# Kernel optimization log

Hardware: AMD Instinct MI355X
Metric: run time of the kernel (lower is better)

The kernel has to match this reference:

```python
import jax, jax.numpy as jnp
import numpy as np

NUM_HEADS = 16  # matches init_kwargs num_heads


def setup_inputs() -> dict:
    key = jax.random.key(0)
    k0, k1, k2, k3, k4 = jax.random.split(key, 5)
    B, p, C = 8, 64, 1024
    N = p * p
    s = 1.0 / np.sqrt(C).astype(np.float32)
    return {
        "x": jax.random.normal(k0, (B, 3, N, C), jnp.float32),
        "wq": jax.random.normal(k1, (C, C), jnp.float32) * s,
        "wk": jax.random.normal(k2, (C, C), jnp.float32) * s,
        "wv": jax.random.normal(k3, (C, C), jnp.float32) * s,
        "w_proj": jax.random.normal(k4, (C, C), jnp.float32) * s,
        "b_proj": jnp.zeros((C,), jnp.float32),
    }


def reference(x, wq, wk, wv, w_proj, b_proj):
    # x: [B, 3, N, C] triplane tokens, N = p*p
    B, G, N, C = x.shape
    p = int(round(N ** 0.5))
    H = NUM_HEADS
    d = C // H
    scale = d ** -0.5

    xg = x.reshape(B, 3, p, p, C)
    # Linear projections are pointwise, so project each plane element once
    # (the torch code redundantly projects gathered copies; math is identical).
    qh = (xg @ wq.T).reshape(B, 3, p, p, H, d)
    kh = (xg @ wk.T).reshape(B, 3, p, p, H, d)
    vh = (xg @ wv.T).reshape(B, 3, p, p, H, d)

    outs = []
    for i in range(3):  # fixed loop over the 3 planes
        q_i = qh[:, i]                       # [B, a, j, H, d] query pixel (a, j)
        k_yz = kh[:, (i + 1) % 3]            # keys: row a of next plane -> [B, a, k, H, d]
        v_yz = vh[:, (i + 1) % 3]
        k_zx = kh[:, (i + 2) % 3]            # keys: column j of other plane -> [B, k, j, H, d]
        v_zx = vh[:, (i + 2) % 3]
        # scores against the p row-keys and p column-keys (2p keys total, 1 query)
        s1 = jnp.einsum('bajhd,bakhd->bajhk', q_i, k_yz) * scale
        s2 = jnp.einsum('bajhd,bkjhd->bajhk', q_i, k_zx) * scale
        attn = jax.nn.softmax(jnp.concatenate([s1, s2], axis=-1), axis=-1)  # [B,a,j,H,2p]
        a1, a2 = attn[..., :p], attn[..., p:]
        o = (jnp.einsum('bajhk,bakhd->bajhd', a1, v_yz)
             + jnp.einsum('bajhk,bkjhd->bajhd', a2, v_zx))  # [B,a,j,H,d]
        outs.append(o.reshape(B, N, C))
    # torch buffer is filled in [plane, B, N] order then reinterpreted as [B,3,N];
    # replicate that reshape quirk faithfully.
    out = jnp.stack(outs, axis=0)            # [3, B, N, C]
    out = out @ w_proj.T + b_proj
    return out.reshape(B, 3, N, C)
```

## Files before the change

kernel.cpp:

```cpp
#include <hip/hip_runtime.h>
#include <hip/hip_bf16.h>
#include <stdint.h>
#include <type_traits>

typedef __hip_bfloat16 hbf16;
typedef short bf16x8 __attribute__((ext_vector_type(8)));
typedef float f32x4 __attribute__((ext_vector_type(4)));
typedef unsigned int u32x4 __attribute__((ext_vector_type(4)));

#define MFMA16(a, b, c) __builtin_amdgcn_mfma_f32_16x16x32_bf16((a), (b), (c), 0, 0, 0)

__device__ __forceinline__ void gload_lds16(const void* g, void* l) {
  __builtin_amdgcn_global_load_lds(
      (const __attribute__((address_space(1))) void*)g,
      (__attribute__((address_space(3))) void*)l, 16, 0, 0);
}

__device__ __forceinline__ float b2f(unsigned short u) {
  union { unsigned int u32; float f; } cv;
  cv.u32 = ((unsigned int)u) << 16;
  return cv.f;
}
__device__ __forceinline__ unsigned short f2b(float f) {
  hbf16 h = __float2bfloat16(f);
  return __builtin_bit_cast(unsigned short, h);
}

__device__ __forceinline__ int swz(int row, int col) {
  return row * 64 + (col ^ ((row & 7) << 3));
}

__global__ __launch_bounds__(256) void cvt_f32_bf16(
    const float* __restrict__ src, unsigned short* __restrict__ dst, long long n)
{
  const long long i0 = ((long long)blockIdx.x * 256 + threadIdx.x) * 8;
  const long long stride = (long long)gridDim.x * 2048;
  for (long long i = i0; i < n; i += stride) {
    const float4 a = *(const float4*)(src + i);
    const float4 b = *(const float4*)(src + i + 4);
    bf16x8 o;
    o[0] = (short)f2b(a.x); o[1] = (short)f2b(a.y);
    o[2] = (short)f2b(a.z); o[3] = (short)f2b(a.w);
    o[4] = (short)f2b(b.x); o[5] = (short)f2b(b.y);
    o[6] = (short)f2b(b.z); o[7] = (short)f2b(b.w);
    *(bf16x8*)(dst + i) = o;
  }
}

__global__ __launch_bounds__(256) void cvt4_w(
    const float* __restrict__ s0, const float* __restrict__ s1,
    const float* __restrict__ s2, const float* __restrict__ s3,
    unsigned short* __restrict__ dst)
{
  const int q = blockIdx.x >> 9;
  const float* src = (q == 0) ? s0 : (q == 1) ? s1 : (q == 2) ? s2 : s3;
  const long long i = ((long long)(blockIdx.x & 511) * 256 + threadIdx.x) * 8;
  const float4 a = *(const float4*)(src + i);
  const float4 b = *(const float4*)(src + i + 4);
  bf16x8 o;
  o[0] = (short)f2b(a.x); o[1] = (short)f2b(a.y);
  o[2] = (short)f2b(a.z); o[3] = (short)f2b(a.w);
  o[4] = (short)f2b(b.x); o[5] = (short)f2b(b.y);
  o[6] = (short)f2b(b.z); o[7] = (short)f2b(b.w);
  *(bf16x8*)(dst + (long long)q * 1048576 + i) = o;
}

__global__ __launch_bounds__(256, 2) void gemm_qkv(
    const unsigned short* __restrict__ A,
    const unsigned short* __restrict__ W,
    unsigned short* __restrict__ Cq,
    unsigned short* __restrict__ Ck,
    unsigned short* __restrict__ Cv,
    int M, int Ntot, int K)
{
  __shared__ __attribute__((aligned(16))) unsigned short Sm[36864];

  const int tid  = threadIdx.x;
  const int lane = tid & 63;
  const int w    = tid >> 6;
  const int wr   = w >> 1;
  const int wc   = w & 1;
  const int lr   = lane & 15;
  const int lg   = lane >> 4;

  const int bx    = blockIdx.x;
  const int xcd   = bx & 7;
  const int idx   = bx >> 3;
  const int tileN = xcd * 3 + idx % 3;
  const int tileM = idx / 3;
  const size_t rowBase = (size_t)tileM * 256;
  const int    colBase = tileN * 128;

  const int sRow   = tid >> 2;
  const int sChunk = (tid & 3) ^ ((tid >> 3) & 3);
  const unsigned short* Ag0 = A + (rowBase +   0 + sRow) * (size_t)K + sChunk * 8;
  const unsigned short* Ag1 = A + (rowBase +  64 + sRow) * (size_t)K + sChunk * 8;
  const unsigned short* Ag2 = A + (rowBase + 128 + sRow) * (size_t)K + sChunk * 8;
  const unsigned short* Ag3 = A + (rowBase + 192 + sRow) * (size_t)K + sChunk * 8;
  const unsigned short* Wg0 = W + ((size_t)colBase +  0 + sRow) * K + sChunk * 8;
  const unsigned short* Wg1 = W + ((size_t)colBase + 64 + sRow) * K + sChunk * 8;

  f32x4 acc[8][4] = {};
  const int nt = K >> 5;

#pragma unroll
  for (int p = 0; p < 2; ++p) {
    const size_t ke = (size_t)p * 32;
    unsigned short* ab = Sm + p * 8192;
    unsigned short* bb = Sm + 24576 + p * 4096;
    gload_lds16(Ag0 + ke, ab +        w * 512);
    gload_lds16(Ag1 + ke, ab + 2048 + w * 512);
    gload_lds16(Ag2 + ke, ab + 4096 + w * 512);
    gload_lds16(Ag3 + ke, ab + 6144 + w * 512);
    gload_lds16(Wg0 + ke, bb +        w * 512);
    gload_lds16(Wg1 + ke, bb + 2048 + w * 512);
  }

#define QITER(T, VM, STG)                                                     \
  do {                                                                        \
    asm volatile("s_waitcnt vmcnt(" VM ")" ::: "memory");                     \
    __builtin_amdgcn_s_barrier();                                             \
    __builtin_amdgcn_sched_barrier(0);                                        \
    if (STG) {                                                                \
      const int nb = ((T) + 2) % 3;                                           \
      const size_t ke = (size_t)((T) + 2) * 32;                               \
      unsigned short* ab = Sm + nb * 8192;                                    \
      unsigned short* bb = Sm + 24576 + nb * 4096;                            \
      gload_lds16(Ag0 + ke, ab +        w * 512);                             \
      gload_lds16(Ag1 + ke, ab + 2048 + w * 512);                             \
      gload_lds16(Ag2 + ke, ab + 4096 + w * 512);                             \
      gload_lds16(Ag3 + ke, ab + 6144 + w * 512);                             \
      gload_lds16(Wg0 + ke, bb +        w * 512);                             \
      gload_lds16(Wg1 + ke, bb + 2048 + w * 512);                             \
    }                                                                         \
    const unsigned short* asb = Sm + ((T) % 3) * 8192;                        \
    const unsigned short* bsb = Sm + 24576 + ((T) % 3) * 4096;                \
    bf16x8 af[8], bfv[4];                                                     \
    _Pragma("unroll")                                                         \
    for (int mi = 0; mi < 8; ++mi) {                                          \
      const int row = wr * 128 + mi * 16 + lr;                                \
      af[mi] = *(const bf16x8*)(asb + row * 32 + (lg ^ ((row >> 1) & 3)) * 8);\
    }                                                                         \
    _Pragma("unroll")                                                         \
    for (int ni = 0; ni < 4; ++ni) {                                          \
      const int row = wc * 64 + ni * 16 + lr;                                 \
      bfv[ni] = *(const bf16x8*)(bsb + row * 32 + (lg ^ ((row >> 1) & 3)) * 8);\
    }                                                                         \
    _Pragma("unroll")                                                         \
    for (int mi = 0; mi < 8; ++mi)                                            \
      _Pragma("unroll")                                                       \
      for (int ni = 0; ni < 4; ++ni)                                          \
        acc[mi][ni] = MFMA16(af[mi], bfv[ni], acc[mi][ni]);                   \
  } while (0)

  for (int t = 0; t < nt - 2; ++t) QITER(t, "6", true);
  QITER(nt - 2, "6", false);
  QITER(nt - 1, "0", false);
#undef QITER

  __syncthreads();
  unsigned short* G = Sm + wr * 16384;
#pragma unroll
  for (int mi = 0; mi < 8; ++mi)
#pragma unroll
    for (int ni = 0; ni < 4; ++ni)
#pragma unroll
      for (int r = 0; r < 4; ++r) {
        const int row = mi * 16 + lg * 4 + r;
        const int c   = wc * 64 + ni * 16 + lr;
        G[row * 128 + (c ^ (((row >> 2) & 3) << 4))] = f2b(acc[mi][ni][r]);
      }
  __syncthreads();

  const int out = colBase >> 10;
  unsigned short* Co = (out == 0) ? Cq : (out == 1) ? Ck : Cv;
  const int colLocal = colBase & 1023;
#pragma unroll
  for (int it = 0; it < 16; ++it) {
    const int ch  = it * 128 + wc * 64 + lane;
    const int row = ch >> 4, cc = ch & 15;
    const u32x4 v = *(const u32x4*)(G + row * 128 + ((cc * 8) ^ (((row >> 2) & 3) << 4)));
    *(u32x4*)(Co + (rowBase + wr * 128 + row) * 1024 + colLocal + cc * 8) = v;
  }
}

template <typename OutT>
__global__ __launch_bounds__(512, 4) void gemm_bt(
    const unsigned short* __restrict__ A,
    const unsigned short* __restrict__ W,
    const float* __restrict__ bias,
    OutT* __restrict__ C,
    int M, int N, int K)
{
  __shared__ __attribute__((aligned(16))) unsigned short Sm[36864];

  const int tid  = threadIdx.x;
  const int lane = tid & 63;
  const int w    = tid >> 6;
  const int wr64 = (w >> 1) * 64;
  const int wc64 = (w & 1) * 64;
  const int lr   = lane & 15;
  const int lg   = lane >> 4;
  const int wofs = w * 512;

  const int nwg     = gridDim.x;
  const int bx      = blockIdx.x;
  const int logical = (bx & 7) * (nwg >> 3) + (bx >> 3);
  const int colsN   = N >> 7;
  const int tileM   = logical / colsN;
  const int tileN   = logical - tileM * colsN;
  const size_t rowBase = (size_t)tileM * 256;
  const int    colBase = tileN * 128;

  const int sRow   = tid >> 2;
  const int sChunk = (tid & 3) ^ ((tid >> 3) & 3);
  const unsigned short* Ag0 = A + (rowBase + sRow) * (size_t)K + sChunk * 8;
  const unsigned short* Ag1 = Ag0 + (size_t)128 * K;
  const unsigned short* Wg0 = W + ((size_t)colBase + sRow) * K + sChunk * 8;

  f32x4 acc[4][4] = {};
  const int nt = K >> 5;

#pragma unroll
  for (int p = 0; p < 2; ++p) {
    const size_t ke = (size_t)p * 32;
    gload_lds16(Ag0 + ke, Sm + p * 8192 + wofs);
    gload_lds16(Ag1 + ke, Sm + p * 8192 + 4096 + wofs);
    gload_lds16(Wg0 + ke, Sm + 24576 + p * 4096 + wofs);
  }

#define GITER(T, VM, STG)                                                     \
  do {                                                                        \
    asm volatile("s_waitcnt vmcnt(" VM ")" ::: "memory");                     \
    __builtin_amdgcn_s_barrier();                                             \
    __builtin_amdgcn_sched_barrier(0);                                        \
    if (STG) {                                                                \
      const int nb = ((T) + 2) % 3;                                           \
      const size_t ke = (size_t)((T) + 2) * 32;                               \
      gload_lds16(Ag0 + ke, Sm + nb * 8192 + wofs);                           \
      gload_lds16(Ag1 + ke, Sm + nb * 8192 + 4096 + wofs);                    \
      gload_lds16(Wg0 + ke, Sm + 24576 + nb * 4096 + wofs);                   \
    }                                                                         \
    const unsigned short* asb = Sm + ((T) % 3) * 8192;                        \
    const unsigned short* bsb = Sm + 24576 + ((T) % 3) * 4096;                \
    bf16x8 af[4], bfv[4];                                                     \
    _Pragma("unroll")                                                         \
    for (int mi = 0; mi < 4; ++mi) {                                          \
      const int row = wr64 + mi * 16 + lr;                                    \
      af[mi] = *(const bf16x8*)(asb + row * 32 + (lg ^ ((row >> 1) & 3)) * 8);\
    }                                                                         \
    _Pragma("unroll")                                                         \
    for (int ni = 0; ni < 4; ++ni) {                                          \
      const int row = wc64 + ni * 16 + lr;                                    \
      bfv[ni] = *(const bf16x8*)(bsb + row * 32 + (lg ^ ((row >> 1) & 3)) * 8);\
    }                                                                         \
    _Pragma("unroll")                                                         \
    for (int mi = 0; mi < 4; ++mi)                                            \
      _Pragma("unroll")                                                       \
      for (int ni = 0; ni < 4; ++ni)                                          \
        acc[mi][ni] = MFMA16(af[mi], bfv[ni], acc[mi][ni]);                   \
  } while (0)

  for (int t = 0; t < nt - 2; ++t) GITER(t, "3", true);
  GITER(nt - 2, "3", false);
  GITER(nt - 1, "0", false);
#undef GITER

  __syncthreads();

  float bv[4];
#pragma unroll
  for (int ni = 0; ni < 4; ++ni)
    bv[ni] = bias ? bias[colBase + wc64 + ni * 16 + lr] : 0.0f;

  const size_t R0 = rowBase + wr64;
  const int    C0 = colBase + wc64;

#pragma unroll
  for (int batch = 0; batch < 2; ++batch) {
    if constexpr (std::is_same_v<OutT, float>) {
      float* reg = (float*)(void*)Sm + w * 2048;
#pragma unroll
      for (int mi2 = 0; mi2 < 2; ++mi2) {
        const int mi = batch * 2 + mi2;
#pragma unroll
        for (int ni = 0; ni < 4; ++ni)
#pragma unroll
          for (int r = 0; r < 4; ++r) {
            const int row = mi2 * 16 + lg * 4 + r;
            reg[row * 64 + ((ni * 16 + lr) ^ (((row >> 2) & 3) << 4))] =
                acc[mi][ni][r] + bv[ni];
          }
      }
      asm volatile("s_waitcnt lgkmcnt(0)" ::: "memory");
      __builtin_amdgcn_sched_barrier(0);
#pragma unroll
      for (int it = 0; it < 8; ++it) {
        const int ch  = it * 64 + lane;
        const int row = ch >> 4, cc = ch & 15;
        const float4 v = *(const float4*)(reg + row * 64 + ((cc * 4) ^ (((row >> 2) & 3) << 4)));
        *(float4*)((float*)C + (R0 + batch * 32 + row) * (size_t)N + C0 + cc * 4) = v;
      }
    } else {
      unsigned short* reg = Sm + w * 2048;
#pragma unroll
      for (int mi2 = 0; mi2 < 2; ++mi2) {
        const int mi = batch * 2 + mi2;
#pragma unroll
        for (int ni = 0; ni < 4; ++ni)
#pragma unroll
          for (int r = 0; r < 4; ++r)
            reg[(mi2 * 16 + lg * 4 + r) * 64 + ni * 16 + lr] =
                f2b(acc[mi][ni][r] + bv[ni]);
      }
      asm volatile("s_waitcnt lgkmcnt(0)" ::: "memory");
      __builtin_amdgcn_sched_barrier(0);
#pragma unroll
      for (int it = 0; it < 4; ++it) {
        const int ch  = it * 64 + lane;
        const int row = ch >> 3, cc = ch & 7;
        const u32x4 v = *(const u32x4*)(reg + row * 64 + cc * 8);
        *(u32x4*)((unsigned short*)C + (R0 + batch * 32 + row) * (size_t)N + C0 + cc * 8) = v;
      }
    }
  }
}

__global__ __launch_bounds__(256) void attn_yz(
    const unsigned short* __restrict__ Q,
    const unsigned short* __restrict__ Kx,
    const unsigned short* __restrict__ Vx,
    unsigned short* __restrict__ O1,
    float* __restrict__ m1s, float* __restrict__ l1s)
{
  __shared__ __attribute__((aligned(16))) unsigned short Qs[4096], Ks[4096], Vs[4096], Ps[4096];

  const int bid = blockIdx.x;
  const int h = bid & 15;
  const int a = (bid >> 4) & 63;
  const int b = (bid >> 10) & 7;
  const int i = bid >> 13;
  const int i1 = (i + 1) % 3;

  const size_t qoff = ((size_t)((b * 3 + i) * 4096 + a * 64)) * 1024 + h * 64;
  const size_t koff = ((size_t)((b * 3 + i1) * 4096 + a * 64)) * 1024 + h * 64;

  const int tid = threadIdx.x;
#pragma unroll
  for (int it = 0; it < 2; ++it) {
    const int idx = it * 2048 + tid * 8;
    const int row = idx >> 6, col = idx & 63;
    const int d = swz(row, col);
    *(bf16x8*)&Qs[d] = *(const bf16x8*)(Q + qoff + (size_t)row * 1024 + col);
    *(bf16x8*)&Ks[d] = *(const bf16x8*)(Kx + koff + (size_t)row * 1024 + col);
    *(bf16x8*)&Vs[d] = *(const bf16x8*)(Vx + koff + (size_t)row * 1024 + col);
  }
  __syncthreads();

  const int lane = tid & 63;
  const int w  = tid >> 6;
  const int lr = lane & 15;
  const int lg = lane >> 4;

  f32x4 sa[4] = {};
  {
    const bf16x8 aq0 = *(const bf16x8*)&Qs[swz(w * 16 + lr, lg * 8)];
    const bf16x8 aq1 = *(const bf16x8*)&Qs[swz(w * 16 + lr, 32 + lg * 8)];
#pragma unroll
    for (int nf = 0; nf < 4; ++nf) {
      const bf16x8 bk0 = *(const bf16x8*)&Ks[swz(nf * 16 + lr, lg * 8)];
      const bf16x8 bk1 = *(const bf16x8*)&Ks[swz(nf * 16 + lr, 32 + lg * 8)];
      sa[nf] = MFMA16(aq0, bk0, sa[nf]);
      sa[nf] = MFMA16(aq1, bk1, sa[nf]);
    }
  }

  const float scale = 0.125f;
  float m[4], ls[4];
#pragma unroll
  for (int r = 0; r < 4; ++r) {
#pragma unroll
    for (int nf = 0; nf < 4; ++nf) sa[nf][r] *= scale;
    float v = fmaxf(fmaxf(sa[0][r], sa[1][r]), fmaxf(sa[2][r], sa[3][r]));
    v = fmaxf(v, __shfl_xor(v, 1));
    v = fmaxf(v, __shfl_xor(v, 2));
    v = fmaxf(v, __shfl_xor(v, 4));
    v = fmaxf(v, __shfl_xor(v, 8));
    m[r] = v;
    float s = 0.0f;
#pragma unroll
    for (int nf = 0; nf < 4; ++nf) { const float p = __expf(sa[nf][r] - v); sa[nf][r] = p; s += p; }
    s += __shfl_xor(s, 1);
    s += __shfl_xor(s, 2);
    s += __shfl_xor(s, 4);
    s += __shfl_xor(s, 8);
    ls[r] = s;
  }

#pragma unroll
  for (int nf = 0; nf < 4; ++nf)
#pragma unroll
    for (int r = 0; r < 4; ++r)
      Ps[swz(w * 16 + lg * 4 + r, nf * 16 + lr)] = f2b(sa[nf][r]);

  if (lr == 0) {
    const size_t sb = ((size_t)(i * 8 + b) * 16 + h) * 4096 + a * 64 + w * 16 + lg * 4;
#pragma unroll
    for (int r = 0; r < 4; ++r) { m1s[sb + r] = m[r]; l1s[sb + r] = ls[r]; }
  }
  __syncthreads();

  f32x4 oa[4] = {};
#pragma unroll
  for (int ks = 0; ks < 2; ++ks) {
    const bf16x8 ap = *(const bf16x8*)&Ps[swz(w * 16 + lr, ks * 32 + lg * 8)];
#pragma unroll
    for (int df = 0; df < 4; ++df) {
      bf16x8 bv;
#pragma unroll
      for (int e = 0; e < 8; ++e)
        bv[e] = (short)Vs[swz(ks * 32 + lg * 8 + e, df * 16 + lr)];
      oa[df] = MFMA16(ap, bv, oa[df]);
    }
  }

  const size_t ob = ((size_t)(i * 8 + b) * 4096 + a * 64) * 1024 + h * 64;
#pragma unroll
  for (int df = 0; df < 4; ++df)
#pragma unroll
    for (int r = 0; r < 4; ++r)
      O1[ob + (size_t)(w * 16 + lg * 4 + r) * 1024 + df * 16 + lr] = f2b(oa[df][r]);
}

__global__ __launch_bounds__(256) void attn_zx(
    const unsigned short* __restrict__ Q,
    const unsigned short* __restrict__ Kx,
    const unsigned short* __restrict__ Vx,
    unsigned short* __restrict__ O1,
    const float* __restrict__ m1s, const float* __restrict__ l1s)
{
  __shared__ __attribute__((aligned(16))) unsigned short Qs[4096], Ks[4096], Vs[4096], Ps[4096];

  const int bid = blockIdx.x;
  const int j = bid & 63;
  const int h = (bid >> 6) & 15;
  const int b = (bid >> 10) & 7;
  const int i = bid >> 13;
  const int i2 = (i + 2) % 3;

  const size_t qoff = ((size_t)(b * 3 + i) * 4096 + j) * 1024 + h * 64;
  const size_t koff = ((size_t)(b * 3 + i2) * 4096 + j) * 1024 + h * 64;
  const size_t rstride = 65536;

  const int tid = threadIdx.x;
#pragma unroll
  for (int it = 0; it < 2; ++it) {
    const int idx = it * 2048 + tid * 8;
    const int row = idx >> 6, col = idx & 63;
    const int d = swz(row, col);
    *(bf16x8*)&Qs[d] = *(const bf16x8*)(Q + qoff + (size_t)row * rstride + col);
    *(bf16x8*)&Ks[d] = *(const bf16x8*)(Kx + koff + (size_t)row * rstride + col);
    *(bf16x8*)&Vs[d] = *(const bf16x8*)(Vx + koff + (size_t)row * rstride + col);
  }
  __syncthreads();

  const int lane = tid & 63;
  const int w  = tid >> 6;
  const int lr = lane & 15;
  const int lg = lane >> 4;

  f32x4 sa[4] = {};
  {
    const bf16x8 aq0 = *(const bf16x8*)&Qs[swz(w * 16 + lr, lg * 8)];
    const bf16x8 aq1 = *(const bf16x8*)&Qs[swz(w * 16 + lr, 32 + lg * 8)];
#pragma unroll
    for (int nf = 0; nf < 4; ++nf) {
      const bf16x8 bk0 = *(const bf16x8*)&Ks[swz(nf * 16 + lr, lg * 8)];
      const bf16x8 bk1 = *(const bf16x8*)&Ks[swz(nf * 16 + lr, 32 + lg * 8)];
      sa[nf] = MFMA16(aq0, bk0, sa[nf]);
      sa[nf] = MFMA16(aq1, bk1, sa[nf]);
    }
  }

  const float scale = 0.125f;
  float m[4], ls[4];
#pragma unroll
  for (int r = 0; r < 4; ++r) {
#pragma unroll
    for (int nf = 0; nf < 4; ++nf) sa[nf][r] *= scale;
    float v = fmaxf(fmaxf(sa[0][r], sa[1][r]), fmaxf(sa[2][r], sa[3][r]));
    v = fmaxf(v, __shfl_xor(v, 1));
    v = fmaxf(v, __shfl_xor(v, 2));
    v = fmaxf(v, __shfl_xor(v, 4));
    v = fmaxf(v, __shfl_xor(v, 8));
    m[r] = v;
    float s = 0.0f;
#pragma unroll
    for (int nf = 0; nf < 4; ++nf) { const float p = __expf(sa[nf][r] - v); sa[nf][r] = p; s += p; }
    s += __shfl_xor(s, 1);
    s += __shfl_xor(s, 2);
    s += __shfl_xor(s, 4);
    s += __shfl_xor(s, 8);
    ls[r] = s;
  }

  float c1[4], c2[4], rden[4];
  const size_t sb = ((size_t)(i * 8 + b) * 16 + h) * 4096 + j;
#pragma unroll
  for (int r = 0; r < 4; ++r) {
    const int arow = w * 16 + lg * 4 + r;
    const float mm1 = m1s[sb + (size_t)arow * 64];
    const float ll1 = l1s[sb + (size_t)arow * 64];
    const float mm = fmaxf(mm1, m[r]);
    const float e1 = __expf(mm1 - mm);
    const float e2 = __expf(m[r] - mm);
    c1[r] = e1; c2[r] = e2;
    rden[r] = 1.0f / (e1 * ll1 + e2 * ls[r]);
  }

#pragma unroll
  for (int nf = 0; nf < 4; ++nf)
#pragma unroll
    for (int r = 0; r < 4; ++r)
      Ps[swz(w * 16 + lg * 4 + r, nf * 16 + lr)] = f2b(sa[nf][r]);
  __syncthreads();

  f32x4 oa[4] = {};
#pragma unroll
  for (int ks = 0; ks < 2; ++ks) {
    const bf16x8 ap = *(const bf16x8*)&Ps[swz(w * 16 + lr, ks * 32 + lg * 8)];
#pragma unroll
    for (int df = 0; df < 4; ++df) {
      bf16x8 bv;
#pragma unroll
      for (int e = 0; e < 8; ++e)
        bv[e] = (short)Vs[swz(ks * 32 + lg * 8 + e, df * 16 + lr)];
      oa[df] = MFMA16(ap, bv, oa[df]);
    }
  }

  const size_t ob = ((size_t)(i * 8 + b) * 4096 + j) * 1024 + h * 64;
#pragma unroll
  for (int df = 0; df < 4; ++df)
#pragma unroll
    for (int r = 0; r < 4; ++r) {
      const size_t addr = ob + (size_t)(w * 16 + lg * 4 + r) * rstride + df * 16 + lr;
      const float o1v = b2f(O1[addr]);
      O1[addr] = f2b((c1[r] * o1v + c2[r] * oa[df][r]) * rden[r]);
    }
}

extern "C" void kernel_launch(void* const* d_in, const int* in_sizes, int n_in,
                              void* d_out, int out_size, void* d_ws, size_t ws_size,
                              hipStream_t stream)
{
  const float* x  = (const float*)d_in[0];
  const float* wq = (const float*)d_in[1];
  const float* wk = (const float*)d_in[2];
  const float* wv = (const float*)d_in[3];
  const float* wp = (const float*)d_in[4];
  const float* bp = (const float*)d_in[5];

  const int M = 98304, N = 1024, K = 1024;
  const size_t SLAB = 201326592ull;
  const size_t STAT = 6291456ull;

  char* ws = (char*)d_ws;
  unsigned short* xb  = (unsigned short*)(ws);
  unsigned short* Kb  = (unsigned short*)(ws + SLAB);
  unsigned short* Vb  = (unsigned short*)(ws + 2 * SLAB);
  float* m1s          = (float*)(ws + 3 * SLAB);
  float* l1s          = (float*)(ws + 3 * SLAB + STAT);
  unsigned short* wqb = (unsigned short*)(ws + 3 * SLAB + 2 * STAT);
  unsigned short* wpb = wqb + 3145728;
  unsigned short* Qb  = (unsigned short*)d_out;
  unsigned short* O1  = xb;

  dim3 blk(256);
  cvt_f32_bf16<<<dim3(4096), blk, 0, stream>>>(x, xb, (long long)M * 1024);
  cvt4_w<<<dim3(2048), blk, 0, stream>>>(wq, wk, wv, wp, wqb);

  gemm_qkv<<<dim3((M / 256) * (3072 / 128)), dim3(256), 0, stream>>>(
      xb, wqb, Qb, Kb, Vb, M, 3072, K);

  attn_yz<<<dim3(24576), blk, 0, stream>>>(Qb, Kb, Vb, O1, m1s, l1s);
  attn_zx<<<dim3(24576), blk, 0, stream>>>(Qb, Kb, Vb, O1, m1s, l1s);

  gemm_bt<float><<<dim3((M / 256) * (N / 128)), dim3(512), 0, stream>>>(
      O1, wpb, bp, (float*)d_out, M, N, K);
}
```

Measured before the change: 1.392 ms.

## Double-buffer GEMMs with smaller LDS and rebuild projection GEMM as 256-thread tile

Both GEMMs go from triple-buffered to double-buffered LDS staging. This shrinks shared memory so three workgroups can fit per CU (launch bounds now 256,3). The epilogues are split into halves or batches so the smaller LDS can still stage output. The projection GEMM is rewritten from a 512-thread 256x128 tile with 4x4 per wave into a 256-thread kernel with 8x4 MFMA tiles per wave, matching the QKV kernel. The trade is shallower prefetch: each iteration now waits on vmcnt(0), so global-load latency is less hidden, in exchange for higher occupancy and more work per wave.

```diff
diff --git a/kernel.cpp b/kernel.cpp
--- a/kernel.cpp
+++ b/kernel.cpp
@@ -65,7 +65,7 @@
   *(bf16x8*)(dst + (long long)q * 1048576 + i) = o;
 }
 
-__global__ __launch_bounds__(256, 2) void gemm_qkv(
+__global__ __launch_bounds__(256, 3) void gemm_qkv(
     const unsigned short* __restrict__ A,
     const unsigned short* __restrict__ W,
     unsigned short* __restrict__ Cq,
@@ -73,7 +73,7 @@
     unsigned short* __restrict__ Cv,
     int M, int Ntot, int K)
 {
-  __shared__ __attribute__((aligned(16))) unsigned short Sm[36864];
+  __shared__ __attribute__((aligned(16))) unsigned short Sm[24576];
 
   const int tid  = threadIdx.x;
   const int lane = tid & 63;
@@ -103,29 +103,27 @@
   f32x4 acc[8][4] = {};
   const int nt = K >> 5;
 
-#pragma unroll
-  for (int p = 0; p < 2; ++p) {
-    const size_t ke = (size_t)p * 32;
-    unsigned short* ab = Sm + p * 8192;
-    unsigned short* bb = Sm + 24576 + p * 4096;
-    gload_lds16(Ag0 + ke, ab +        w * 512);
-    gload_lds16(Ag1 + ke, ab + 2048 + w * 512);
-    gload_lds16(Ag2 + ke, ab + 4096 + w * 512);
-    gload_lds16(Ag3 + ke, ab + 6144 + w * 512);
-    gload_lds16(Wg0 + ke, bb +        w * 512);
-    gload_lds16(Wg1 + ke, bb + 2048 + w * 512);
-  }
-
-#define QITER(T, VM, STG)                                                     \
+  {
+    unsigned short* ab = Sm;
+    unsigned short* bb = Sm + 16384;
+    gload_lds16(Ag0, ab +        w * 512);
+    gload_lds16(Ag1, ab + 2048 + w * 512);
+    gload_lds16(Ag2, ab + 4096 + w * 512);
+    gload_lds16(Ag3, ab + 6144 + w * 512);
+    gload_lds16(Wg0, bb +        w * 512);
+    gload_lds16(Wg1, bb + 2048 + w * 512);
+  }
+
+#define QITER(T, STG)                                                         \
   do {                                                                        \
-    asm volatile("s_waitcnt vmcnt(" VM ")" ::: "memory");                     \
+    asm volatile("s_waitcnt vmcnt(0)" ::: "memory");                          \
     __builtin_amdgcn_s_barrier();                                             \
     __builtin_amdgcn_sched_barrier(0);                                        \
     if (STG) {                                                                \
-      const int nb = ((T) + 2) % 3;                                           \
-      const size_t ke = (size_t)((T) + 2) * 32;                               \
+      const int nb = ((T) + 1) & 1;                                           \
+      const size_t ke = (size_t)((T) + 1) * 32;                               \
       unsigned short* ab = Sm + nb * 8192;                                    \
-      unsigned short* bb = Sm + 24576 + nb * 4096;                            \
+      unsigned short* bb = Sm + 16384 + nb * 4096;                            \
       gload_lds16(Ag0 + ke, ab +        w * 512);                             \
       gload_lds16(Ag1 + ke, ab + 2048 + w * 512);                             \
       gload_lds16(Ag2 + ke, ab + 4096 + w * 512);                             \
@@ -133,8 +131,8 @@
       gload_lds16(Wg0 + ke, bb +        w * 512);                             \
       gload_lds16(Wg1 + ke, bb + 2048 + w * 512);                             \
     }                                                                         \
-    const unsigned short* asb = Sm + ((T) % 3) * 8192;                        \
-    const unsigned short* bsb = Sm + 24576 + ((T) % 3) * 4096;                \
+    const unsigned short* asb = Sm + ((T) & 1) * 8192;                        \
+    const unsigned short* bsb = Sm + 16384 + ((T) & 1) * 4096;                \
     bf16x8 af[8], bfv[4];                                                     \
     _Pragma("unroll")                                                         \
     for (int mi = 0; mi < 8; ++mi) {                                          \
@@ -153,55 +151,58 @@
         acc[mi][ni] = MFMA16(af[mi], bfv[ni], acc[mi][ni]);                   \
   } while (0)
 
-  for (int t = 0; t < nt - 2; ++t) QITER(t, "6", true);
-  QITER(nt - 2, "6", false);
-  QITER(nt - 1, "0", false);
+  for (int t = 0; t < nt - 1; ++t) QITER(t, true);
+  QITER(nt - 1, false);
 #undef QITER
 
   __syncthreads();
-  unsigned short* G = Sm + wr * 16384;
-#pragma unroll
-  for (int mi = 0; mi < 8; ++mi)
-#pragma unroll
-    for (int ni = 0; ni < 4; ++ni)
-#pragma unroll
-      for (int r = 0; r < 4; ++r) {
-        const int row = mi * 16 + lg * 4 + r;
-        const int c   = wc * 64 + ni * 16 + lr;
-        G[row * 128 + (c ^ (((row >> 2) & 3) << 4))] = f2b(acc[mi][ni][r]);
-      }
-  __syncthreads();
-
   const int out = colBase >> 10;
   unsigned short* Co = (out == 0) ? Cq : (out == 1) ? Ck : Cv;
   const int colLocal = colBase & 1023;
-#pragma unroll
-  for (int it = 0; it < 16; ++it) {
-    const int ch  = it * 128 + wc * 64 + lane;
-    const int row = ch >> 4, cc = ch & 15;
-    const u32x4 v = *(const u32x4*)(G + row * 128 + ((cc * 8) ^ (((row >> 2) & 3) << 4)));
-    *(u32x4*)(Co + (rowBase + wr * 128 + row) * 1024 + colLocal + cc * 8) = v;
-  }
-}
-
-template <typename OutT>
-__global__ __launch_bounds__(512, 4) void gemm_bt(
+  unsigned short* G = Sm + wr * 8192;
+
+#pragma unroll
+  for (int half = 0; half < 2; ++half) {
+#pragma unroll
+    for (int mi2 = 0; mi2 < 4; ++mi2) {
+      const int mi = half * 4 + mi2;
+#pragma unroll
+      for (int ni = 0; ni < 4; ++ni)
+#pragma unroll
+        for (int r = 0; r < 4; ++r) {
+          const int row = mi2 * 16 + lg * 4 + r;
+          const int c   = wc * 64 + ni * 16 + lr;
+          G[row * 128 + (c ^ (((row >> 2) & 3) << 4))] = f2b(acc[mi][ni][r]);
+        }
+    }
+    __syncthreads();
+#pragma unroll
+    for (int it = 0; it < 8; ++it) {
+      const int ch  = it * 128 + wc * 64 + lane;
+      const int row = ch >> 4, cc = ch & 15;
+      const u32x4 v = *(const u32x4*)(G + row * 128 + ((cc * 8) ^ (((row >> 2) & 3) << 4)));
+      *(u32x4*)(Co + (rowBase + wr * 128 + half * 64 + row) * 1024 + colLocal + cc * 8) = v;
+    }
+    __syncthreads();
+  }
+}
+
+__global__ __launch_bounds__(256, 3) void gemm_proj(
     const unsigned short* __restrict__ A,
     const unsigned short* __restrict__ W,
     const float* __restrict__ bias,
-    OutT* __restrict__ C,
+    float* __restrict__ C,
     int M, int N, int K)
 {
-  __shared__ __attribute__((aligned(16))) unsigned short Sm[36864];
+  __shared__ __attribute__((aligned(16))) unsigned short Sm[24576];
 
   const int tid  = threadIdx.x;
   const int lane = tid & 63;
   const int w    = tid >> 6;
-  const int wr64 = (w >> 1) * 64;
-  const int wc64 = (w & 1) * 64;
+  const int wr   = w >> 1;
+  const int wc   = w & 1;
   const int lr   = lane & 15;
   const int lg   = lane >> 4;
-  const int wofs = w * 512;
 
   const int nwg     = gridDim.x;
   const int bx      = blockIdx.x;
@@ -214,115 +215,100 @@
 
   const int sRow   = tid >> 2;
   const int sChunk = (tid & 3) ^ ((tid >> 3) & 3);
-  const unsigned short* Ag0 = A + (rowBase + sRow) * (size_t)K + sChunk * 8;
-  const unsigned short* Ag1 = Ag0 + (size_t)128 * K;
-  const unsigned short* Wg0 = W + ((size_t)colBase + sRow) * K + sChunk * 8;
-
-  f32x4 acc[4][4] = {};
+  const unsigned short* Ag0 = A + (rowBase +   0 + sRow) * (size_t)K + sChunk * 8;
+  const unsigned short* Ag1 = A + (rowBase +  64 + sRow) * (size_t)K + sChunk * 8;
+  const unsigned short* Ag2 = A + (rowBase + 128 + sRow) * (size_t)K + sChunk * 8;
+  const unsigned short* Ag3 = A + (rowBase + 192 + sRow) * (size_t)K + sChunk * 8;
+  const unsigned short* Wg0 = W + ((size_t)colBase +  0 + sRow) * K + sChunk * 8;
+  const unsigned short* Wg1 = W + ((size_t)colBase + 64 + sRow) * K + sChunk * 8;
+
+  f32x4 acc[8][4] = {};
   const int nt = K >> 5;
 
-#pragma unroll
-  for (int p = 0; p < 2; ++p) {
-    const size_t ke = (size_t)p * 32;
-    gload_lds16(Ag0 + ke, Sm + p * 8192 + wofs);
-    gload_lds16(Ag1 + ke, Sm + p * 8192 + 4096 + wofs);
-    gload_lds16(Wg0 + ke, Sm + 24576 + p * 4096 + wofs);
-  }
-
-#define GITER(T, VM, STG)                                                     \
+  {
+    unsigned short* ab = Sm;
+    unsigned short* bb = Sm + 16384;
+    gload_lds16(Ag0, ab +        w * 512);
+    gload_lds16(Ag1, ab + 2048 + w * 512);
+    gload_lds16(Ag2, ab + 4096 + w * 512);
+    gload_lds16(Ag3, ab + 6144 + w * 512);
+    gload_lds16(Wg0, bb +        w * 512);
+    gload_lds16(Wg1, bb + 2048 + w * 512);
+  }
+
+#define PITER(T, STG)                                                         \
   do {                                                                        \
-    asm volatile("s_waitcnt vmcnt(" VM ")" ::: "memory");                     \
+    asm volatile("s_waitcnt vmcnt(0)" ::: "memory");                          \
     __builtin_amdgcn_s_barrier();                                             \
     __builtin_amdgcn_sched_barrier(0);                                        \
     if (STG) {                                                                \
-      const int nb = ((T) + 2) % 3;                                           \
-      const size_t ke = (size_t)((T) + 2) * 32;                               \
-      gload_lds16(Ag0 + ke, Sm + nb * 8192 + wofs);                           \
-      gload_lds16(Ag1 + ke, Sm + nb * 8192 + 4096 + wofs);                    \
-      gload_lds16(Wg0 + ke, Sm + 24576 + nb * 4096 + wofs);                   \
+      const int nb = ((T) + 1) & 1;                                           \
+      const size_t ke = (size_t)((T) + 1) * 32;                               \
+      unsigned short* ab = Sm + nb * 8192;                                    \
+      unsigned short* bb = Sm + 16384 + nb * 4096;                            \
+      gload_lds16(Ag0 + ke, ab +        w * 512);                             \
+      gload_lds16(Ag1 + ke, ab + 2048 + w * 512);                             \
+      gload_lds16(Ag2 + ke, ab + 4096 + w * 512);                             \
+      gload_lds16(Ag3 + ke, ab + 6144 + w * 512);                             \
+      gload_lds16(Wg0 + ke, bb +        w * 512);                             \
+      gload_lds16(Wg1 + ke, bb + 2048 + w * 512);                             \
     }                                                                         \
-    const unsigned short* asb = Sm + ((T) % 3) * 8192;                        \
-    const unsigned short* bsb = Sm + 24576 + ((T) % 3) * 4096;                \
-    bf16x8 af[4], bfv[4];                                                     \
+    const unsigned short* asb = Sm + ((T) & 1) * 8192;                        \
+    const unsigned short* bsb = Sm + 16384 + ((T) & 1) * 4096;                \
+    bf16x8 af[8], bfv[4];                                                     \
     _Pragma("unroll")                                                         \
-    for (int mi = 0; mi < 4; ++mi) {                                          \
-      const int row = wr64 + mi * 16 + lr;                                    \
+    for (int mi = 0; mi < 8; ++mi) {                                          \
+      const int row = wr * 128 + mi * 16 + lr;                                \
       af[mi] = *(const bf16x8*)(asb + row * 32 + (lg ^ ((row >> 1) & 3)) * 8);\
     }                                                                         \
     _Pragma("unroll")                                                         \
     for (int ni = 0; ni < 4; ++ni) {                                          \
-      const int row = wc64 + ni * 16 + lr;                                    \
+      const int row = wc * 64 + ni * 16 + lr;                                 \
       bfv[ni] = *(const bf16x8*)(bsb + row * 32 + (lg ^ ((row >> 1) & 3)) * 8);\
     }                                                                         \
     _Pragma("unroll")                                                         \
-    for (int mi = 0; mi < 4; ++mi)                                            \
+    for (int mi = 0; mi < 8; ++mi)                                            \
       _Pragma("unroll")                                                       \
       for (int ni = 0; ni < 4; ++ni)                                          \
         acc[mi][ni] = MFMA16(af[mi], bfv[ni], acc[mi][ni]);                   \
   } while (0)
 
-  for (int t = 0; t < nt - 2; ++t) GITER(t, "3", true);
-  GITER(nt - 2, "3", false);
-  GITER(nt - 1, "0", false);
-#undef GITER
+  for (int t = 0; t < nt - 1; ++t) PITER(t, true);
+  PITER(nt - 1, false);
+#undef PITER
 
   __syncthreads();
 
   float bv[4];
 #pragma unroll
   for (int ni = 0; ni < 4; ++ni)
-    bv[ni] = bias ? bias[colBase + wc64 + ni * 16 + lr] : 0.0f;
-
-  const size_t R0 = rowBase + wr64;
-  const int    C0 = colBase + wc64;
-
-#pragma unroll
-  for (int batch = 0; batch < 2; ++batch) {
-    if constexpr (std::is_same_v<OutT, float>) {
-      float* reg = (float*)(void*)Sm + w * 2048;
-#pragma unroll
-      for (int mi2 = 0; mi2 < 2; ++mi2) {
-        const int mi = batch * 2 + mi2;
-#pragma unroll
-        for (int ni = 0; ni < 4; ++ni)
-#pragma unroll
-          for (int r = 0; r < 4; ++r) {
-            const int row = mi2 * 16 + lg * 4 + r;
-            reg[row * 64 + ((ni * 16 + lr) ^ (((row >> 2) & 3) << 4))] =
-                acc[mi][ni][r] + bv[ni];
-          }
-      }
-      asm volatile("s_waitcnt lgkmcnt(0)" ::: "memory");
-      __builtin_amdgcn_sched_barrier(0);
-#pragma unroll
-      for (int it = 0; it < 8; ++it) {
-        const int ch  = it * 64 + lane;
-        const int row = ch >> 4, cc = ch & 15;
-        const float4 v = *(const float4*)(reg + row * 64 + ((cc * 4) ^ (((row >> 2) & 3) << 4)));
-        *(float4*)((float*)C + (R0 + batch * 32 + row) * (size_t)N + C0 + cc * 4) = v;
-      }
-    } else {
-      unsigned short* reg = Sm + w * 2048;
-#pragma unroll
-      for (int mi2 = 0; mi2 < 2; ++mi2) {
-        const int mi = batch * 2 + mi2;
-#pragma unroll
-        for (int ni = 0; ni < 4; ++ni)
-#pragma unroll
-          for (int r = 0; r < 4; ++r)
-            reg[(mi2 * 16 + lg * 4 + r) * 64 + ni * 16 + lr] =
-                f2b(acc[mi][ni][r] + bv[ni]);
-      }
-      asm volatile("s_waitcnt lgkmcnt(0)" ::: "memory");
-      __builtin_amdgcn_sched_barrier(0);
-#pragma unroll
-      for (int it = 0; it < 4; ++it) {
-        const int ch  = it * 64 + lane;
-        const int row = ch >> 3, cc = ch & 7;
-        const u32x4 v = *(const u32x4*)(reg + row * 64 + cc * 8);
-        *(u32x4*)((unsigned short*)C + (R0 + batch * 32 + row) * (size_t)N + C0 + cc * 8) = v;
-      }
-    }
+    bv[ni] = bias ? bias[colBase + wc * 64 + ni * 16 + lr] : 0.0f;
+
+  float* G = (float*)(void*)Sm + wr * 4096;
+
+#pragma unroll
+  for (int batch = 0; batch < 4; ++batch) {
+#pragma unroll
+    for (int mi2 = 0; mi2 < 2; ++mi2) {
+      const int mi = batch * 2 + mi2;
+#pragma unroll
+      for (int ni = 0; ni < 4; ++ni)
+#pragma unroll
+        for (int r = 0; r < 4; ++r) {
+          const int row = mi2 * 16 + lg * 4 + r;
+          const int c   = wc * 64 + ni * 16 + lr;
+          G[row * 128 + (c ^ (((row >> 2) & 3) << 4))] = acc[mi][ni][r] + bv[ni];
+        }
+    }
+    __syncthreads();
+#pragma unroll
+    for (int it = 0; it < 8; ++it) {
+      const int ch  = it * 128 + wc * 64 + lane;
+      const int row = ch >> 5, cc = ch & 31;
+      const float4 v = *(const float4*)(G + row * 128 + ((cc * 4) ^ (((row >> 2) & 3) << 4)));
+      *(float4*)(C + (rowBase + wr * 128 + batch * 32 + row) * (size_t)N + colBase + cc * 4) = v;
+    }
+    __syncthreads();
   }
 }
 
@@ -586,6 +572,6 @@
   attn_yz<<<dim3(24576), blk, 0, stream>>>(Qb, Kb, Vb, O1, m1s, l1s);
   attn_zx<<<dim3(24576), blk, 0, stream>>>(Qb, Kb, Vb, O1, m1s, l1s);
 
-  gemm_bt<float><<<dim3((M / 256) * (N / 128)), dim3(512), 0, stream>>>(
+  gemm_proj<<<dim3((M / 256) * (N / 128)), dim3(256), 0, stream>>>(
       O1, wpb, bp, (float*)d_out, M, N, K);
 }
```

New measurement: 1.422 ms. 2.2% more time.
